# Performance work log

Measured on AMD Instinct MI355X. Metric: run time of the kernel, lower is better.

## Reference

```python
import jax, jax.numpy as jnp
import numpy as np

N = 100000   # nodes
E = 1200000  # edges
D = 64       # feat_dim == num_hidden
G = 64       # graphs in batch
EPS = 1e-5   # BatchNorm eps


def setup_inputs() -> dict:
    key = jax.random.key(0)
    ks = jax.random.split(key, 24)
    inp = {}
    inp['x'] = jax.random.normal(ks[0], (N, D), jnp.float32)
    inp['edge_index'] = jax.random.randint(ks[1], (2, E), 0, N, dtype=jnp.int32)
    inp['batch'] = jnp.sort(jax.random.randint(ks[2], (N,), 0, G, dtype=jnp.int32))
    s = 1.0 / np.sqrt(D)
    for i, kw in zip(range(1, 4), ks[3:6]):
        inp[f'W{i}'] = jax.random.normal(kw, (D, D), jnp.float32) * s
    for i, kb in zip(range(1, 4), ks[6:9]):
        inp[f'b{i}'] = jax.random.normal(kb, (D,), jnp.float32) * 0.02
    for i, base in zip(range(1, 3), (9, 13)):
        inp[f'g{i}'] = 1.0 + 0.1 * jax.random.normal(ks[base], (D,), jnp.float32)
        inp[f'be{i}'] = 0.1 * jax.random.normal(ks[base + 1], (D,), jnp.float32)
        inp[f'rm{i}'] = 0.1 * jax.random.normal(ks[base + 2], (D,), jnp.float32)
        inp[f'rv{i}'] = jax.random.uniform(ks[base + 3], (D,), jnp.float32, 0.5, 1.5)
    return inp


def _gcn_conv(x, W, b, src, dst, n):
    # PyG GCNConv: h = X W; symmetric normalization with self-loops; scatter-add; + bias
    h = x @ W
    deg = jax.ops.segment_sum(jnp.ones((src.shape[0],), h.dtype), dst, num_segments=n) + 1.0
    dis = jax.lax.rsqrt(deg)                          # deg >= 1 from self loop
    msg = (dis[src] * dis[dst])[:, None] * h[src]     # [E, D] gather + normalize
    out = jax.ops.segment_sum(msg, dst, num_segments=n)
    out = out + (dis * dis)[:, None] * h              # self-loop contribution
    return out + b


def _bn(x, g, be, rm, rv):
    # BatchNorm1d in eval mode (running stats)
    return (x - rm) * jax.lax.rsqrt(rv + EPS) * g + be


def reference(x, edge_index, batch, W1, b1, W2, b2, W3, b3,
              g1, be1, rm1, rv1, g2, be2, rm2, rv2):
    src, dst = edge_index[0], edge_index[1]
    h = jax.nn.relu(_bn(_gcn_conv(x, W1, b1, src, dst, N), g1, be1, rm1, rv1))
    h = jax.nn.relu(_bn(_gcn_conv(h, W2, b2, src, dst, N), g2, be2, rm2, rv2))
    h = _gcn_conv(h, W3, b3, src, dst, N)
    # global mean pool over graphs
    counts = jax.ops.segment_sum(jnp.ones((N,), h.dtype), batch, num_segments=G)
    sums = jax.ops.segment_sum(h, batch, num_segments=G)
    hg = sums / jnp.maximum(counts, 1.0)[:, None]
    return (h, hg)
```

## Files before the change

### kernel.cpp

```cpp
#include <hip/hip_runtime.h>
#include <hip/hip_fp16.h>

#define D 64
#define EPS 1e-5f

#define BK_SHIFT 9
#define BK_W 512
#define NBMAX 256
#define BK_CAP 8192
#define CHUNK 4096

typedef _Float16 h8v __attribute__((ext_vector_type(8)));
typedef float f4v __attribute__((ext_vector_type(4)));


__global__ __launch_bounds__(256) void bucket_k(const int* __restrict__ src,
                                                const int* __restrict__ dst,
                                                int* __restrict__ bcnt,
                                                int* __restrict__ pairs,
                                                int e, int nbk) {
  __shared__ int hcnt[NBMAX];
  __shared__ int hbase[NBMAX];
  const int t = threadIdx.x;
  const int e0 = blockIdx.x * CHUNK;
  const int e1 = min(e0 + CHUNK, e);
  for (int i = t; i < nbk; i += 256) hcnt[i] = 0;
  __syncthreads();
  for (int i = e0 + t; i < e1; i += 256)
    atomicAdd(&hcnt[dst[i] >> BK_SHIFT], 1);
  __syncthreads();
  for (int i = t; i < nbk; i += 256) {
    int c = hcnt[i];
    hbase[i] = c ? atomicAdd(&bcnt[i], c) : 0;
    hcnt[i] = 0;
  }
  __syncthreads();
  for (int i = e0 + t; i < e1; i += 256) {
    int s = src[i], d = dst[i];
    int b = d >> BK_SHIFT;
    int r = hbase[b] + atomicAdd(&hcnt[b], 1);
    if (r < BK_CAP) pairs[(size_t)b * BK_CAP + r] = (s << BK_SHIFT) | (d & (BK_W - 1));
  }
}


__global__ __launch_bounds__(256) void bucket2csr_k(const int* __restrict__ bcnt,
                                                    const int* __restrict__ pairs,
                                                    int2* __restrict__ rpdeg,
                                                    float* __restrict__ dis,
                                                    int* __restrict__ col, int n) {
  __shared__ int h[BK_W];
  __shared__ int cur[BK_W];
  __shared__ int s1[256], s2[256];
  __shared__ int stage[BK_CAP];
  const int b = blockIdx.x, t = threadIdx.x;
  const int base = b << BK_SHIFT;
  const int slab0 = b * BK_CAP;
  const int m = min(bcnt[b], BK_CAP);

  h[t] = 0; h[t + 256] = 0;
  for (int i = t; i < BK_CAP; i += 256) stage[i] = 0;
  __syncthreads();
  const int* p = pairs + (size_t)b * BK_CAP;
  for (int i = t; i < m; i += 256) atomicAdd(&h[p[i] & (BK_W - 1)], 1);
  __syncthreads();

  const int pc1 = (h[t] + 3) & ~3;
  const int pc2 = (h[t + 256] + 3) & ~3;
  s1[t] = pc1; s2[t] = pc2;
  __syncthreads();
  for (int off = 1; off < 256; off <<= 1) {
    int x1 = (t >= off) ? s1[t - off] : 0;
    int x2 = (t >= off) ? s2[t - off] : 0;
    __syncthreads();
    s1[t] += x1; s2[t] += x2;
    __syncthreads();
  }
  const int tot1 = s1[255];
  const int mpad = tot1 + s2[255];
  cur[t]       = s1[t] - pc1;
  cur[t + 256] = tot1 + s2[t] - pc2;
  {
    int n1 = base + t, n2 = base + t + 256;
    if (n1 < n) { rpdeg[n1] = make_int2(slab0 + cur[t], h[t]);
                  dis[n1] = rsqrtf((float)h[t] + 1.0f); }
    if (n2 < n) { rpdeg[n2] = make_int2(slab0 + cur[t + 256], h[t + 256]);
                  dis[n2] = rsqrtf((float)h[t + 256] + 1.0f); }
  }
  __syncthreads();

  for (int i = t; i < m; i += 256) {
    int pk = p[i];
    int r = atomicAdd(&cur[pk & (BK_W - 1)], 1);
    stage[r] = pk >> BK_SHIFT;
  }
  __syncthreads();
  const int mout = min(mpad + 16, BK_CAP);
  for (int i = t; i < mout; i += 256) col[slab0 + i] = stage[i];
}


__global__ __launch_bounds__(256) void setup_k(const float* __restrict__ W1,
                                               const float* __restrict__ W2,
                                               const float* __restrict__ W3,
                                               const float* __restrict__ b1,
                                               const float* __restrict__ b2,
                                               const float* __restrict__ b3,
                                               const float* __restrict__ g1, const float* __restrict__ be1,
                                               const float* __restrict__ rm1, const float* __restrict__ rv1,
                                               const float* __restrict__ g2, const float* __restrict__ be2,
                                               const float* __restrict__ rm2, const float* __restrict__ rv2,
                                               _Float16* __restrict__ Wt1,
                                               _Float16* __restrict__ Wt2,
                                               _Float16* __restrict__ Wt3,
                                               float* __restrict__ scsh,
                                               int* __restrict__ zbase, int zwords,
                                               unsigned int* __restrict__ hzrow) {
  int gid = blockIdx.x * 256 + threadIdx.x;
  if (gid < zwords) { zbase[gid] = 0; return; }
  gid -= zwords;
  if (gid < 32) { hzrow[gid] = 0u; return; }
  gid -= 32;
  if (gid < 192) {
    int j = gid & 63, l = gid >> 6;
    float sc, sh;
    if (l == 0)      { sc = g1[j] * rsqrtf(rv1[j] + EPS); sh = (b1[j] - rm1[j]) * sc + be1[j]; }
    else if (l == 1) { sc = g2[j] * rsqrtf(rv2[j] + EPS); sh = (b2[j] - rm2[j]) * sc + be2[j]; }
    else             { sc = 1.0f;                          sh = b3[j]; }
    scsh[l * 128 + j] = sc;
    scsh[l * 128 + 64 + j] = sh;
    return;
  }
  gid -= 192;
  if (gid < 3 * 4096) {
    const int mat = gid >> 12, e = gid & 4095;
    const float* Wm = (mat == 0) ? W1 : (mat == 1) ? W2 : W3;
    _Float16* Wt    = (mat == 0) ? Wt1 : (mat == 1) ? Wt2 : Wt3;
    const int k = e >> 6, j = e & 63;
    Wt[j * 64 + k] = (_Float16)Wm[e];
  }
}


template <typename InT>
__global__ __launch_bounds__(256) void gemm_k(const InT* __restrict__ in,
                                              const _Float16* __restrict__ Wt,
                                              const float* __restrict__ dis,
                                              __half* __restrict__ out, int nrows) {
  const int lane = threadIdx.x & 63;
  const int w    = threadIdx.x >> 6;
  const int t16  = lane & 15;
  const int q    = lane >> 4;
  const int rb   = blockIdx.x * 64 + w * 16;
  if (rb >= nrows) return;

  h8v bf[4][2];
#pragma unroll
  for (int cg = 0; cg < 4; ++cg) {
    const _Float16* wp = Wt + (cg * 16 + t16) * 64 + q * 8;
    bf[cg][0] = *(const h8v*)(wp);
    bf[cg][1] = *(const h8v*)(wp + 32);
  }

  const int ar = min(rb + t16, nrows - 1);
  h8v a0, a1;
  if constexpr (sizeof(InT) == 2) {
    const _Float16* ap = (const _Float16*)in + (size_t)ar * D + q * 8;
    a0 = *(const h8v*)(ap);
    a1 = *(const h8v*)(ap + 32);
  } else {
    const float* ap = (const float*)in + (size_t)ar * D + q * 8;
    const float4 l0 = *(const float4*)(ap);
    const float4 h0 = *(const float4*)(ap + 4);
    const float4 l1 = *(const float4*)(ap + 32);
    const float4 h1 = *(const float4*)(ap + 36);
    a0[0] = (_Float16)l0.x; a0[1] = (_Float16)l0.y; a0[2] = (_Float16)l0.z; a0[3] = (_Float16)l0.w;
    a0[4] = (_Float16)h0.x; a0[5] = (_Float16)h0.y; a0[6] = (_Float16)h0.z; a0[7] = (_Float16)h0.w;
    a1[0] = (_Float16)l1.x; a1[1] = (_Float16)l1.y; a1[2] = (_Float16)l1.z; a1[3] = (_Float16)l1.w;
    a1[4] = (_Float16)h1.x; a1[5] = (_Float16)h1.y; a1[6] = (_Float16)h1.z; a1[7] = (_Float16)h1.w;
  }

  f4v acc0 = {0.f, 0.f, 0.f, 0.f};
  f4v acc1 = acc0, acc2 = acc0, acc3 = acc0;
  acc0 = __builtin_amdgcn_mfma_f32_16x16x32_f16(a0, bf[0][0], acc0, 0, 0, 0);
  acc1 = __builtin_amdgcn_mfma_f32_16x16x32_f16(a0, bf[1][0], acc1, 0, 0, 0);
  acc2 = __builtin_amdgcn_mfma_f32_16x16x32_f16(a0, bf[2][0], acc2, 0, 0, 0);
  acc3 = __builtin_amdgcn_mfma_f32_16x16x32_f16(a0, bf[3][0], acc3, 0, 0, 0);
  acc0 = __builtin_amdgcn_mfma_f32_16x16x32_f16(a1, bf[0][1], acc0, 0, 0, 0);
  acc1 = __builtin_amdgcn_mfma_f32_16x16x32_f16(a1, bf[1][1], acc1, 0, 0, 0);
  acc2 = __builtin_amdgcn_mfma_f32_16x16x32_f16(a1, bf[2][1], acc2, 0, 0, 0);
  acc3 = __builtin_amdgcn_mfma_f32_16x16x32_f16(a1, bf[3][1], acc3, 0, 0, 0);

  const float4 dv = *(const float4*)&dis[rb + q * 4];
  _Float16* oh = (_Float16*)out;
#pragma unroll
  for (int r = 0; r < 4; ++r) {
    const int row = rb + q * 4 + r;
    if (row < nrows) {
      const float dsc = (&dv.x)[r];
      _Float16* op = oh + (size_t)row * D + t16;
      op[0]  = (_Float16)(dsc * acc0[r]);
      op[16] = (_Float16)(dsc * acc1[r]);
      op[32] = (_Float16)(dsc * acc2[r]);
      op[48] = (_Float16)(dsc * acc3[r]);
    }
  }
}


template <bool RELU, typename OutT>
__global__ __launch_bounds__(256) void agg_k(const __half* __restrict__ h2s,
                                             const int2* __restrict__ rpdeg,
                                             const int* __restrict__ col,
                                             const float* __restrict__ dis,
                                             const float* __restrict__ scsh,
                                             OutT* __restrict__ out, int n) {
  const int lane = threadIdx.x & 63;
  const int wv   = (blockIdx.x * blockDim.x + threadIdx.x) >> 6;
  const int nb   = __builtin_amdgcn_readfirstlane(wv * 4);
  if (nb >= n) return;
  const int g  = lane >> 4;
  const int sl = lane & 15;
  const int jb = 4 * g;
  const uint2* __restrict__ h2v = (const uint2*)h2s;

  int nd[4], p[4], dg[4];
#pragma unroll
  for (int i = 0; i < 4; ++i) nd[i] = min(nb + i, n - 1);
#pragma unroll
  for (int i = 0; i < 4; ++i) { int2 rd = rpdeg[nd[i]]; p[i] = rd.x; dg[i] = rd.y; }

  uint2 self[4];
  int4  cc[4];
#pragma unroll
  for (int i = 0; i < 4; ++i) {
    self[i] = h2v[(size_t)nd[i] * 16 + sl];
    cc[i]   = *(const int4*)&col[p[i] + jb];
  }

  const __half2 zero2 = __floats2half2_rn(0.f, 0.f);
  const uint2 zz = make_uint2(0u, 0u);
  __half2 acc[4][4];
#pragma unroll
  for (int i = 0; i < 4; ++i)
#pragma unroll
    for (int s = 0; s < 4; ++s) acc[i][s] = zero2;

#pragma unroll
  for (int i = 0; i < 4; ++i) {
    uint2 r0 = h2v[(size_t)cc[i].x * 16 + sl];
    uint2 r1 = h2v[(size_t)cc[i].y * 16 + sl];
    uint2 r2 = h2v[(size_t)cc[i].z * 16 + sl];
    uint2 r3 = h2v[(size_t)cc[i].w * 16 + sl];
    r0 = (jb + 0 < dg[i]) ? r0 : zz;  r1 = (jb + 1 < dg[i]) ? r1 : zz;
    r2 = (jb + 2 < dg[i]) ? r2 : zz;  r3 = (jb + 3 < dg[i]) ? r3 : zz;
    acc[i][0] = __hadd2(acc[i][0], *(const __half2*)&r0.x);
    acc[i][1] = __hadd2(acc[i][1], *(const __half2*)&r0.y);
    acc[i][2] = __hadd2(acc[i][2], *(const __half2*)&r1.x);
    acc[i][3] = __hadd2(acc[i][3], *(const __half2*)&r1.y);
    acc[i][0] = __hadd2(acc[i][0], *(const __half2*)&r2.x);
    acc[i][1] = __hadd2(acc[i][1], *(const __half2*)&r2.y);
    acc[i][2] = __hadd2(acc[i][2], *(const __half2*)&r3.x);
    acc[i][3] = __hadd2(acc[i][3], *(const __half2*)&r3.y);
  }

#pragma unroll
  for (int i = 0; i < 4; ++i) {
    for (int e = 16; e < dg[i]; e += 16) {
      const int4 c2 = *(const int4*)&col[p[i] + e + jb];
      uint2 r0 = h2v[(size_t)c2.x * 16 + sl];
      uint2 r1 = h2v[(size_t)c2.y * 16 + sl];
      uint2 r2 = h2v[(size_t)c2.z * 16 + sl];
      uint2 r3 = h2v[(size_t)c2.w * 16 + sl];
      const int j = e + jb;
      r0 = (j + 0 < dg[i]) ? r0 : zz;  r1 = (j + 1 < dg[i]) ? r1 : zz;
      r2 = (j + 2 < dg[i]) ? r2 : zz;  r3 = (j + 3 < dg[i]) ? r3 : zz;
      acc[i][0] = __hadd2(acc[i][0], *(const __half2*)&r0.x);
      acc[i][1] = __hadd2(acc[i][1], *(const __half2*)&r0.y);
      acc[i][2] = __hadd2(acc[i][2], *(const __half2*)&r1.x);
      acc[i][3] = __hadd2(acc[i][3], *(const __half2*)&r1.y);
      acc[i][0] = __hadd2(acc[i][0], *(const __half2*)&r2.x);
      acc[i][1] = __hadd2(acc[i][1], *(const __half2*)&r2.y);
      acc[i][2] = __hadd2(acc[i][2], *(const __half2*)&r3.x);
      acc[i][3] = __hadd2(acc[i][3], *(const __half2*)&r3.y);
    }
  }

  const float4 sc = *(const float4*)&scsh[4 * sl];
  const float4 sh = *(const float4*)&scsh[64 + 4 * sl];

#pragma unroll
  for (int i = 0; i < 4; ++i) {
    const float2 a0 = __half22float2(acc[i][0]);
    const float2 a1 = __half22float2(acc[i][1]);
    const float2 a2 = __half22float2(acc[i][2]);
    const float2 a3 = __half22float2(acc[i][3]);
    const float2 s0f = __half22float2(*(const __half2*)&self[i].x);
    const float2 s1f = __half22float2(*(const __half2*)&self[i].y);
    float r0 = (a0.x + a2.x) + (g == 0 ? s0f.x : 0.f);
    float r1 = (a0.y + a2.y) + (g == 0 ? s0f.y : 0.f);
    float r2 = (a1.x + a3.x) + (g == 0 ? s1f.x : 0.f);
    float r3 = (a1.y + a3.y) + (g == 0 ? s1f.y : 0.f);
    r0 += __shfl_xor(r0, 16, 64); r1 += __shfl_xor(r1, 16, 64);
    r2 += __shfl_xor(r2, 16, 64); r3 += __shfl_xor(r3, 16, 64);
    r0 += __shfl_xor(r0, 32, 64); r1 += __shfl_xor(r1, 32, 64);
    r2 += __shfl_xor(r2, 32, 64); r3 += __shfl_xor(r3, 32, 64);
    const float di = dis[nd[i]];
    float o0 = fmaf(di * r0, sc.x, sh.x);
    float o1 = fmaf(di * r1, sc.y, sh.y);
    float o2 = fmaf(di * r2, sc.z, sh.z);
    float o3 = fmaf(di * r3, sc.w, sh.w);
    if (RELU) {
      o0 = fmaxf(o0, 0.f); o1 = fmaxf(o1, 0.f);
      o2 = fmaxf(o2, 0.f); o3 = fmaxf(o3, 0.f);
    }
    if (g == 0 && nb + i < n) {
      if constexpr (sizeof(OutT) == 2) {
        union { __half2 h[2]; uint2 u; } v;
        v.h[0] = __floats2half2_rn(o0, o1);
        v.h[1] = __floats2half2_rn(o2, o3);
        *(uint2*)&out[(size_t)nd[i] * D + 4 * sl] = v.u;
      } else {
        *(float4*)&out[(size_t)nd[i] * D + 4 * sl] = make_float4(o0, o1, o2, o3);
      }
    }
  }
}


__global__ __launch_bounds__(256) void pool_k(const float* __restrict__ h,
                                              const int* __restrict__ batch,
                                              float* __restrict__ psum,
                                              float* __restrict__ pcnt, int n) {
  int lane  = threadIdx.x & 63;
  int wid   = __builtin_amdgcn_readfirstlane((blockIdx.x * blockDim.x + threadIdx.x) >> 6);
  int start = wid * 64;
  if (start >= n) return;
  int end = min(start + 64, n);
  int cur = batch[start];
  float sum = 0.f;
  int run = 0;
  for (int i = start; i < end; ++i) {
    int g = batch[i];
    if (g != cur) {
      atomicAdd(&psum[cur * D + lane], sum);
      if (lane == 0) atomicAdd(&pcnt[cur], (float)run);
      sum = 0.f; run = 0; cur = g;
    }
    sum += h[(size_t)i * D + lane];
    run += 1;
  }
  atomicAdd(&psum[cur * D + lane], sum);
  if (lane == 0) atomicAdd(&pcnt[cur], (float)run);
}

__global__ void pooldiv_k(const float* __restrict__ psum, const float* __restrict__ pcnt,
                          float* __restrict__ hg) {
  int t = blockIdx.x * blockDim.x + threadIdx.x;
  if (t < 64 * D) hg[t] = psum[t] / fmaxf(pcnt[t >> 6], 1.0f);
}


extern "C" void kernel_launch(void* const* d_in, const int* in_sizes, int n_in,
                              void* d_out, int out_size, void* d_ws, size_t ws_size,
                              hipStream_t stream) {
  const float* x   = (const float*)d_in[0];
  const int*   ei  = (const int*)d_in[1];
  const int*   bat = (const int*)d_in[2];
  const float* W1  = (const float*)d_in[3];
  const float* W2  = (const float*)d_in[4];
  const float* W3  = (const float*)d_in[5];
  const float* b1  = (const float*)d_in[6];
  const float* b2  = (const float*)d_in[7];
  const float* b3  = (const float*)d_in[8];
  const float* g1  = (const float*)d_in[9];
  const float* be1 = (const float*)d_in[10];
  const float* rm1 = (const float*)d_in[11];
  const float* rv1 = (const float*)d_in[12];
  const float* g2  = (const float*)d_in[13];
  const float* be2 = (const float*)d_in[14];
  const float* rm2 = (const float*)d_in[15];
  const float* rv2 = (const float*)d_in[16];

  const int n = in_sizes[0] / D;
  const int e = in_sizes[1] / 2;
  const int* src = ei;
  const int* dst = ei + e;
  const int nbk = (n + BK_W - 1) >> BK_SHIFT;

  char* ws = (char*)d_ws;
  size_t off = 0;
  auto alloc = [&](size_t bytes) -> void* {
    void* p = ws + off;
    off = (off + bytes + 255) & ~(size_t)255;
    return p;
  };
  __half*   buf16 = (__half*)alloc((size_t)n * D * 2);
  int*      pairs = (int*)alloc((size_t)NBMAX * BK_CAP * 4);
  __half*   hbuf  = (__half*)alloc((size_t)(n + 1) * D * 2);
  int2*     rpdeg = (int2*)alloc((size_t)(n + 1) * 8);
  float*    dis   = (float*)alloc((size_t)(n + 16) * 4);
  int*      col   = (int*)alloc((size_t)NBMAX * BK_CAP * 4);
  float*    scsh  = (float*)alloc(6 * 64 * 4);
  _Float16* Wt1   = (_Float16*)alloc(4096 * 2);
  _Float16* Wt2   = (_Float16*)alloc(4096 * 2);
  _Float16* Wt3   = (_Float16*)alloc(4096 * 2);
  int*      bcnt  = (int*)alloc(NBMAX * 4);
  float*    psum  = (float*)alloc(64 * D * 4);
  float*    pcnt  = (float*)alloc(64 * 4);
  const int zwords = (int)((((char*)pcnt + 64 * 4) - (char*)bcnt) / 4);

  float* hout = (float*)d_out;
  float* hg   = (float*)d_out + (size_t)n * D;

  const int setup_items = zwords + 32 + 192 + 3 * 4096;
  setup_k<<<(setup_items + 255) / 256, 256, 0, stream>>>(
      W1, W2, W3, b1, b2, b3, g1, be1, rm1, rv1, g2, be2, rm2, rv2,
      Wt1, Wt2, Wt3, scsh, bcnt, zwords, (unsigned int*)(hbuf + (size_t)n * D));

  bucket_k<<<(e + CHUNK - 1) / CHUNK, 256, 0, stream>>>(src, dst, bcnt, pairs, e, nbk);
  bucket2csr_k<<<nbk, 256, 0, stream>>>(bcnt, pairs, rpdeg, dis, col, n);

  const int gemm_blocks = (n + 63) / 64;
  const int agg_waves   = (n + 3) / 4;
  const int agg_blocks  = (agg_waves * 64 + 255) / 256;

  gemm_k<float><<<gemm_blocks, 256, 0, stream>>>(x, Wt1, dis, hbuf, n);
  agg_k<true, __half><<<agg_blocks, 256, 0, stream>>>(hbuf, rpdeg, col, dis, scsh + 0 * 128, buf16, n);
  gemm_k<__half><<<gemm_blocks, 256, 0, stream>>>(buf16, Wt2, dis, hbuf, n);
  agg_k<true, __half><<<agg_blocks, 256, 0, stream>>>(hbuf, rpdeg, col, dis, scsh + 1 * 128, buf16, n);
  gemm_k<__half><<<gemm_blocks, 256, 0, stream>>>(buf16, Wt3, dis, hbuf, n);
  agg_k<false, float><<<agg_blocks, 256, 0, stream>>>(hbuf, rpdeg, col, dis, scsh + 2 * 128, hout, n);

  const int pool_waves = (n + 63) / 64;
  pool_k<<<(pool_waves * 64 + 255) / 256, 256, 0, stream>>>(hout, bat, psum, pcnt, n);
  pooldiv_k<<<(64 * D + 255) / 256, 256, 0, stream>>>(psum, pcnt, hg);
}
```

Baseline: 297.7 us.

## Fuse aggregation with next layer's GEMM into one kernel per layer

Adds aggemm_k, which gathers and normalizes neighbour features for 16 nodes per block, applies BN/ReLU, stages the result in LDS, then multiplies by the next layer's weight with MFMA and writes the pre-scaled fp16 output. This replaces two agg+gemm kernel pairs and removes the intermediate buf16 write and re-read plus two launches. Ping-pong hbufA/hbufB buffers are used, and each gets a zeroed padding row. Risk: the 16-node blocks and the block-wide sync may hurt gather latency hiding, and dis is read past n via float4 (the buffer is padded).

Result: faster. 278.7 us (-6.4%).

```diff
diff --git a/kernel.cpp b/kernel.cpp
--- a/kernel.cpp
+++ b/kernel.cpp
@@ -115,12 +115,16 @@
                                                _Float16* __restrict__ Wt3,
                                                float* __restrict__ scsh,
                                                int* __restrict__ zbase, int zwords,
-                                               unsigned int* __restrict__ hzrow) {
+                                               unsigned int* __restrict__ hzrowA,
+                                               unsigned int* __restrict__ hzrowB) {
   int gid = blockIdx.x * 256 + threadIdx.x;
   if (gid < zwords) { zbase[gid] = 0; return; }
   gid -= zwords;
-  if (gid < 32) { hzrow[gid] = 0u; return; }
-  gid -= 32;
+  if (gid < 64) {
+    if (gid < 32) hzrowA[gid] = 0u; else hzrowB[gid - 32] = 0u;
+    return;
+  }
+  gid -= 64;
   if (gid < 192) {
     int j = gid & 63, l = gid >> 6;
     float sc, sh;
@@ -328,6 +332,148 @@
 }
 
 
+template <bool RELU>
+__global__ __launch_bounds__(256) void aggemm_k(const __half* __restrict__ h2s,
+                                                const int2* __restrict__ rpdeg,
+                                                const int* __restrict__ col,
+                                                const float* __restrict__ dis,
+                                                const float* __restrict__ scsh,
+                                                const _Float16* __restrict__ Wt,
+                                                __half* __restrict__ out, int n) {
+  __shared__ _Float16 ylds[16][72];
+  const int lane = threadIdx.x & 63;
+  const int w    = threadIdx.x >> 6;
+  const int nb   = __builtin_amdgcn_readfirstlane(blockIdx.x * 16 + w * 4);
+  const int g  = lane >> 4;
+  const int sl = lane & 15;
+  const int jb = 4 * g;
+  const uint2* __restrict__ h2v = (const uint2*)h2s;
+
+  int nd[4], p[4], dg[4];
+#pragma unroll
+  for (int i = 0; i < 4; ++i) nd[i] = min(nb + i, n - 1);
+#pragma unroll
+  for (int i = 0; i < 4; ++i) { int2 rd = rpdeg[nd[i]]; p[i] = rd.x; dg[i] = rd.y; }
+
+  uint2 self[4];
+  int4  cc[4];
+#pragma unroll
+  for (int i = 0; i < 4; ++i) {
+    self[i] = h2v[(size_t)nd[i] * 16 + sl];
+    cc[i]   = *(const int4*)&col[p[i] + jb];
+  }
+
+  const __half2 zero2 = __floats2half2_rn(0.f, 0.f);
+  const uint2 zz = make_uint2(0u, 0u);
+  __half2 acc[4][4];
+#pragma unroll
+  for (int i = 0; i < 4; ++i)
+#pragma unroll
+    for (int s = 0; s < 4; ++s) acc[i][s] = zero2;
+
+#pragma unroll
+  for (int i = 0; i < 4; ++i) {
+    uint2 r0 = h2v[(size_t)cc[i].x * 16 + sl];
+    uint2 r1 = h2v[(size_t)cc[i].y * 16 + sl];
+    uint2 r2 = h2v[(size_t)cc[i].z * 16 + sl];
+    uint2 r3 = h2v[(size_t)cc[i].w * 16 + sl];
+    r0 = (jb + 0 < dg[i]) ? r0 : zz;  r1 = (jb + 1 < dg[i]) ? r1 : zz;
+    r2 = (jb + 2 < dg[i]) ? r2 : zz;  r3 = (jb + 3 < dg[i]) ? r3 : zz;
+    acc[i][0] = __hadd2(acc[i][0], *(const __half2*)&r0.x);
+    acc[i][1] = __hadd2(acc[i][1], *(const __half2*)&r0.y);
+    acc[i][2] = __hadd2(acc[i][2], *(const __half2*)&r1.x);
+    acc[i][3] = __hadd2(acc[i][3], *(const __half2*)&r1.y);
+    acc[i][0] = __hadd2(acc[i][0], *(const __half2*)&r2.x);
+    acc[i][1] = __hadd2(acc[i][1], *(const __half2*)&r2.y);
+    acc[i][2] = __hadd2(acc[i][2], *(const __half2*)&r3.x);
+    acc[i][3] = __hadd2(acc[i][3], *(const __half2*)&r3.y);
+  }
+
+#pragma unroll
+  for (int i = 0; i < 4; ++i) {
+    for (int e = 16; e < dg[i]; e += 16) {
+      const int4 c2 = *(const int4*)&col[p[i] + e + jb];
+      uint2 r0 = h2v[(size_t)c2.x * 16 + sl];
+      uint2 r1 = h2v[(size_t)c2.y * 16 + sl];
+      uint2 r2 = h2v[(size_t)c2.z * 16 + sl];
+      uint2 r3 = h2v[(size_t)c2.w * 16 + sl];
+      const int j = e + jb;
+      r0 = (j + 0 < dg[i]) ? r0 : zz;  r1 = (j + 1 < dg[i]) ? r1 : zz;
+      r2 = (j + 2 < dg[i]) ? r2 : zz;  r3 = (j + 3 < dg[i]) ? r3 : zz;
+      acc[i][0] = __hadd2(acc[i][0], *(const __half2*)&r0.x);
+      acc[i][1] = __hadd2(acc[i][1], *(const __half2*)&r0.y);
+      acc[i][2] = __hadd2(acc[i][2], *(const __half2*)&r1.x);
+      acc[i][3] = __hadd2(acc[i][3], *(const __half2*)&r1.y);
+      acc[i][0] = __hadd2(acc[i][0], *(const __half2*)&r2.x);
+      acc[i][1] = __hadd2(acc[i][1], *(const __half2*)&r2.y);
+      acc[i][2] = __hadd2(acc[i][2], *(const __half2*)&r3.x);
+      acc[i][3] = __hadd2(acc[i][3], *(const __half2*)&r3.y);
+    }
+  }
+
+  const float4 sc = *(const float4*)&scsh[4 * sl];
+  const float4 sh = *(const float4*)&scsh[64 + 4 * sl];
+
+#pragma unroll
+  for (int i = 0; i < 4; ++i) {
+    const float2 a0 = __half22float2(acc[i][0]);
+    const float2 a1 = __half22float2(acc[i][1]);
+    const float2 a2 = __half22float2(acc[i][2]);
+    const float2 a3 = __half22float2(acc[i][3]);
+    const float2 s0f = __half22float2(*(const __half2*)&self[i].x);
+    const float2 s1f = __half22float2(*(const __half2*)&self[i].y);
+    float r0 = (a0.x + a2.x) + (g == 0 ? s0f.x : 0.f);
+    float r1 = (a0.y + a2.y) + (g == 0 ? s0f.y : 0.f);
+    float r2 = (a1.x + a3.x) + (g == 0 ? s1f.x : 0.f);
+    float r3 = (a1.y + a3.y) + (g == 0 ? s1f.y : 0.f);
+    r0 += __shfl_xor(r0, 16, 64); r1 += __shfl_xor(r1, 16, 64);
+    r2 += __shfl_xor(r2, 16, 64); r3 += __shfl_xor(r3, 16, 64);
+    r0 += __shfl_xor(r0, 32, 64); r1 += __shfl_xor(r1, 32, 64);
+    r2 += __shfl_xor(r2, 32, 64); r3 += __shfl_xor(r3, 32, 64);
+    const float di = dis[nd[i]];
+    float o0 = fmaf(di * r0, sc.x, sh.x);
+    float o1 = fmaf(di * r1, sc.y, sh.y);
+    float o2 = fmaf(di * r2, sc.z, sh.z);
+    float o3 = fmaf(di * r3, sc.w, sh.w);
+    if (RELU) {
+      o0 = fmaxf(o0, 0.f); o1 = fmaxf(o1, 0.f);
+      o2 = fmaxf(o2, 0.f); o3 = fmaxf(o3, 0.f);
+    }
+    if (g == 0) {
+      union { __half2 h[2]; uint2 u; } v;
+      v.h[0] = __floats2half2_rn(o0, o1);
+      v.h[1] = __floats2half2_rn(o2, o3);
+      *(uint2*)&ylds[w * 4 + i][4 * sl] = v.u;
+    }
+  }
+
+  __syncthreads();
+
+  {
+    const h8v a0 = *(const h8v*)&ylds[sl][g * 8];
+    const h8v a1 = *(const h8v*)&ylds[sl][g * 8 + 32];
+    const _Float16* wp = Wt + (w * 16 + sl) * 64 + g * 8;
+    const h8v b0 = *(const h8v*)(wp);
+    const h8v b1 = *(const h8v*)(wp + 32);
+    f4v ga = {0.f, 0.f, 0.f, 0.f};
+    ga = __builtin_amdgcn_mfma_f32_16x16x32_f16(a0, b0, ga, 0, 0, 0);
+    ga = __builtin_amdgcn_mfma_f32_16x16x32_f16(a1, b1, ga, 0, 0, 0);
+
+    const int rb = blockIdx.x * 16;
+    const float4 dv = *(const float4*)&dis[rb + g * 4];
+    _Float16* oh = (_Float16*)out;
+#pragma unroll
+    for (int r = 0; r < 4; ++r) {
+      const int row = rb + g * 4 + r;
+      if (row < n) {
+        const float dsc = (&dv.x)[r];
+        oh[(size_t)row * D + w * 16 + sl] = (_Float16)(dsc * ga[r]);
+      }
+    }
+  }
+}
+
+
 __global__ __launch_bounds__(256) void pool_k(const float* __restrict__ h,
                                               const int* __restrict__ batch,
                                               float* __restrict__ psum,
@@ -395,9 +541,9 @@
     off = (off + bytes + 255) & ~(size_t)255;
     return p;
   };
-  __half*   buf16 = (__half*)alloc((size_t)n * D * 2);
+  __half*   hbufB = (__half*)alloc((size_t)(n + 1) * D * 2);
   int*      pairs = (int*)alloc((size_t)NBMAX * BK_CAP * 4);
-  __half*   hbuf  = (__half*)alloc((size_t)(n + 1) * D * 2);
+  __half*   hbufA = (__half*)alloc((size_t)(n + 1) * D * 2);
   int2*     rpdeg = (int2*)alloc((size_t)(n + 1) * 8);
   float*    dis   = (float*)alloc((size_t)(n + 16) * 4);
   int*      col   = (int*)alloc((size_t)NBMAX * BK_CAP * 4);
@@ -413,24 +559,25 @@
   float* hout = (float*)d_out;
   float* hg   = (float*)d_out + (size_t)n * D;
 
-  const int setup_items = zwords + 32 + 192 + 3 * 4096;
+  const int setup_items = zwords + 64 + 192 + 3 * 4096;
   setup_k<<<(setup_items + 255) / 256, 256, 0, stream>>>(
       W1, W2, W3, b1, b2, b3, g1, be1, rm1, rv1, g2, be2, rm2, rv2,
-      Wt1, Wt2, Wt3, scsh, bcnt, zwords, (unsigned int*)(hbuf + (size_t)n * D));
+      Wt1, Wt2, Wt3, scsh, bcnt, zwords,
+      (unsigned int*)(hbufA + (size_t)n * D),
+      (unsigned int*)(hbufB + (size_t)n * D));
 
   bucket_k<<<(e + CHUNK - 1) / CHUNK, 256, 0, stream>>>(src, dst, bcnt, pairs, e, nbk);
   bucket2csr_k<<<nbk, 256, 0, stream>>>(bcnt, pairs, rpdeg, dis, col, n);
 
   const int gemm_blocks = (n + 63) / 64;
+  const int fuse_blocks = (n + 15) / 16;
   const int agg_waves   = (n + 3) / 4;
   const int agg_blocks  = (agg_waves * 64 + 255) / 256;
 
-  gemm_k<float><<<gemm_blocks, 256, 0, stream>>>(x, Wt1, dis, hbuf, n);
-  agg_k<true, __half><<<agg_blocks, 256, 0, stream>>>(hbuf, rpdeg, col, dis, scsh + 0 * 128, buf16, n);
-  gemm_k<__half><<<gemm_blocks, 256, 0, stream>>>(buf16, Wt2, dis, hbuf, n);
-  agg_k<true, __half><<<agg_blocks, 256, 0, stream>>>(hbuf, rpdeg, col, dis, scsh + 1 * 128, buf16, n);
-  gemm_k<__half><<<gemm_blocks, 256, 0, stream>>>(buf16, Wt3, dis, hbuf, n);
-  agg_k<false, float><<<agg_blocks, 256, 0, stream>>>(hbuf, rpdeg, col, dis, scsh + 2 * 128, hout, n);
+  gemm_k<float><<<gemm_blocks, 256, 0, stream>>>(x, Wt1, dis, hbufA, n);
+  aggemm_k<true><<<fuse_blocks, 256, 0, stream>>>(hbufA, rpdeg, col, dis, scsh + 0 * 128, Wt2, hbufB, n);
+  aggemm_k<true><<<fuse_blocks, 256, 0, stream>>>(hbufB, rpdeg, col, dis, scsh + 1 * 128, Wt3, hbufA, n);
+  agg_k<false, float><<<agg_blocks, 256, 0, stream>>>(hbufA, rpdeg, col, dis, scsh + 2 * 128, hout, n);
 
   const int pool_waves = (n + 63) / 64;
   pool_k<<<(pool_waves * 64 + 255) / 256, 256, 0, stream>>>(hout, bat, psum, pcnt, n);
```
